# Kernel optimization log

Hardware: AMD Instinct MI355X
Metric: run time of the kernel (lower is better)

The kernel has to match this reference:

```python
import jax, jax.numpy as jnp
import numpy as np

N = 8192
IN_DIM = 512
OUT_DIM = 512


def setup_inputs() -> dict:
    key = jax.random.key(0)
    kA, kX, k1, k2, k3, k4 = jax.random.split(key, 6)
    A = jax.random.uniform(kA, (N, N), dtype=jnp.float32)  # strictly positive -> nonzero triu
    X = jax.random.normal(kX, (N, IN_DIM), dtype=jnp.float32)
    s = 1.0 / np.sqrt(IN_DIM)
    W1 = jax.random.uniform(k1, (OUT_DIM, IN_DIM), minval=-s, maxval=s, dtype=jnp.float32)  # fc
    b1 = jax.random.uniform(k2, (OUT_DIM,), minval=-s, maxval=s, dtype=jnp.float32)
    W2 = jax.random.uniform(k3, (OUT_DIM, IN_DIM), minval=-s, maxval=s, dtype=jnp.float32)  # fc2
    b2 = jax.random.uniform(k4, (OUT_DIM,), minval=-s, maxval=s, dtype=jnp.float32)
    return {"A": A, "X": X, "W1": W1, "b1": b1, "W2": W2, "b2": b2}


def reference(A, X, W1, b1, W2, b2):
    n = A.shape[0]
    # strictly upper-triangular mask (diagonal=1); with uniform(0,1) fill all these
    # entries are nonzero, so torch.nonzero selects exactly them: m = n(n-1)/2 values.
    triu_mask = jnp.triu(jnp.ones((n, n), dtype=bool), k=1)
    m = n * (n - 1) // 2
    # torch.median = lower median = sorted[(m-1)//2]; pad non-triu entries with +inf
    vals = jnp.where(triu_mask, A, jnp.inf).reshape(-1)
    median_value = jnp.sort(vals)[(m - 1) // 2]
    # A[A < median] = 0
    A_thr = jnp.where(A < median_value, jnp.zeros((), A.dtype), A)
    A_norm = jax.nn.softmax(A_thr, axis=-1)
    fcX = X @ W1.T + b1    # [N, out_dim]
    fc2X = X @ W2.T + b2   # [N, out_dim]
    out = jax.nn.leaky_relu(0.1 * fc2X + 0.9 * (A_norm @ fcX), negative_slope=0.01)
    return out
```

## Files before the change

kernel.cpp:

```cpp
#include <hip/hip_runtime.h>

#define DEVI __device__ __forceinline__

typedef __attribute__((ext_vector_type(8))) short short8;
typedef __attribute__((ext_vector_type(4))) float f32x4;

static constexpr int NN = 8192;
static constexpr int DD = 512;
static constexpr unsigned LOB = 0x3EFE0000u;
static constexpr unsigned HIB = 0x3F020000u;
static constexpr long long K_RANK = 16775167LL;

static constexpr size_t WS_HIST   = 0;
static constexpr size_t WS_CNT    = 1048576;
static constexpr size_t WS_MED    = 1048832;
static constexpr size_t WS_COARSE = 1049088;
static constexpr size_t WS_XB     = 2097152;
static constexpr size_t WS_W1B  = WS_XB  + (size_t)NN * DD * 2;
static constexpr size_t WS_W2B  = WS_W1B + (size_t)DD * DD * 2;
static constexpr size_t WS_FCXT = WS_W2B + (size_t)DD * DD * 2;
static constexpr size_t WS_FC2  = WS_FCXT + (size_t)NN * DD * 2;
static constexpr size_t WS_UP   = WS_FC2 + (size_t)NN * DD * 4;
static constexpr size_t WS_ZP   = WS_UP  + (size_t)4 * NN * DD * 2;

DEVI unsigned short f2bf(float f) {
  unsigned u = __float_as_uint(f);
  u += 0x7fffu + ((u >> 16) & 1u);
  return (unsigned short)(u >> 16);
}
DEVI float bf2f(unsigned short h) { return __uint_as_float(((unsigned)h) << 16); }
DEVI int swz(int row, int kq) { return kq ^ ((row >> 1) & 3); }

DEVI void gl_lds16(const void* g, void* l) {
  __builtin_amdgcn_global_load_lds(
      (const __attribute__((address_space(1))) unsigned*)g,
      (__attribute__((address_space(3))) unsigned*)l, 16, 0, 0);
}

#define VMCNT(n) asm volatile("s_waitcnt vmcnt(" #n ")" ::: "memory")
#define LGKM0 asm volatile("s_waitcnt lgkmcnt(0)" ::: "memory")

__global__ __launch_bounds__(256) void zero_k(uint4* __restrict__ hist4,
                                              unsigned* __restrict__ cntmed) {
  hist4[blockIdx.x * 256 + threadIdx.x] = (uint4){0u, 0u, 0u, 0u};
  if (blockIdx.x == 0 && threadIdx.x < 2) cntmed[threadIdx.x * 64] = 0u;
}


DEVI void convert_body(const float* __restrict__ X, const float* __restrict__ W1,
                       const float* __restrict__ W2, unsigned short* __restrict__ Xb,
                       unsigned short* __restrict__ W1b, unsigned short* __restrict__ W2b,
                       int cb, int tid) {
  const long long NX = (long long)NN * DD;
  const long long NW = (long long)DD * DD;
  const long long total4 = (NX + 2 * NW) / 4;
  for (long long q = (long long)cb * 512 + tid; q < total4; q += 65536LL) {
    long long e = q << 2;
    const float4* src; unsigned short* dst; long long off;
    if (e < NX)           { src = (const float4*)X;  dst = Xb;  off = e; }
    else if (e < NX + NW) { src = (const float4*)W1; dst = W1b; off = e - NX; }
    else                  { src = (const float4*)W2; dst = W2b; off = e - NX - NW; }
    float4 v = src[off >> 2];
    ushort4 o;
    o.x = f2bf(v.x); o.y = f2bf(v.y); o.z = f2bf(v.z); o.w = f2bf(v.w);
    *(ushort4*)(dst + off) = o;
  }
}

DEVI void hist_body(const float* __restrict__ A, unsigned* __restrict__ hist,
                    unsigned* __restrict__ below, int hb, int tid) {
  unsigned cnt = 0;
  const float4* A4 = (const float4*)A;
  const long long STR = 458752LL;
#pragma unroll 1
  for (long long q0 = (long long)hb * 512 + tid; q0 < 16777216LL; q0 += 8 * STR) {
    float4 v[8];
    int act = 0;
#pragma unroll
    for (int i = 0; i < 8; ++i) {
      long long qi = q0 + i * STR;
      if (qi < 16777216LL) {
        int row = (int)(qi >> 11);
        int col = (int)((qi & 2047) << 2);
        if (col + 3 > row) { act |= 1 << i; v[i] = A4[qi]; }
      }
    }
#pragma unroll
    for (int i = 0; i < 8; ++i) {
      if (act & (1 << i)) {
        long long qi = q0 + i * STR;
        int row = (int)(qi >> 11);
        int col = (int)((qi & 2047) << 2);
        float vv[4] = {v[i].x, v[i].y, v[i].z, v[i].w};
#pragma unroll
        for (int j = 0; j < 4; ++j) {
          if (col + j > row) {
            unsigned u = __float_as_uint(vv[j]);
            if (u < LOB) cnt++;
            else if (u < HIB) atomicAdd(&hist[u - LOB], 1u);
          }
        }
      }
    }
  }
  for (int off = 32; off > 0; off >>= 1) cnt += __shfl_down(cnt, off);
  if ((tid & 63) == 0 && cnt) atomicAdd(below, cnt);
}

__global__ __launch_bounds__(512) void stage1_k(const float* __restrict__ A,
                                                const float* __restrict__ X,
                                                const float* __restrict__ W1,
                                                const float* __restrict__ W2,
                                                unsigned* __restrict__ hist,
                                                unsigned* __restrict__ below,
                                                unsigned short* __restrict__ Xb,
                                                unsigned short* __restrict__ W1b,
                                                unsigned short* __restrict__ W2b) {
  const int bx = blockIdx.x;
  if (bx < 128) convert_body(X, W1, W2, Xb, W1b, W2b, bx, threadIdx.x);
  else          hist_body(A, hist, below, bx - 128, threadIdx.x);
}


template <bool BROW, bool OBF>
DEVI void gemm_small_body(const unsigned short* __restrict__ Am,
                          const unsigned short* __restrict__ Bm,
                          const float* __restrict__ bias, void* __restrict__ outp,
                          int ldout, int m0, int n0, char* apB, char* btB) {
  const int tid = threadIdx.x, lane = tid & 63, w = tid >> 6;
  const int wm = w >> 2, wn = w & 3;
  const int lr = lane & 15, lq = lane >> 4;
  const int rL = lane >> 2, kq = lane & 3;
  f32x4 acc[2][4];
#pragma unroll
  for (int i = 0; i < 2; ++i)
#pragma unroll
    for (int j = 0; j < 4; ++j) acc[i][j] = (f32x4){0.f, 0.f, 0.f, 0.f};

#pragma unroll 1
  for (int kt = 0; kt < 16; ++kt) {
    const int k0 = kt * 32;
    __syncthreads();
    if (w < 4) {
      int r = w * 16 + rL;
      gl_lds16(Am + ((size_t)(m0 + r) * DD + k0 + swz(r, kq) * 8), apB + w * 1024);
    }
#pragma unroll
    for (int i = 0; i < 2; ++i) {
      int blk = w * 2 + i;
      int r = blk * 16 + rL;
      gl_lds16(Bm + ((size_t)(n0 + r) * DD + k0 + swz(r, kq) * 8), btB + blk * 1024);
    }
    __syncthreads();
    short8 a[2], b[4];
#pragma unroll
    for (int fr = 0; fr < 2; ++fr) {
      int r = wm * 32 + fr * 16 + lr;
      a[fr] = *(const short8*)(apB + r * 64 + swz(r, lq) * 16);
    }
#pragma unroll
    for (int fc = 0; fc < 4; ++fc) {
      int r = wn * 64 + fc * 16 + lr;
      b[fc] = *(const short8*)(btB + r * 64 + swz(r, lq) * 16);
    }
#pragma unroll
    for (int fr = 0; fr < 2; ++fr)
#pragma unroll
      for (int fc = 0; fc < 4; ++fc)
        acc[fr][fc] = __builtin_amdgcn_mfma_f32_16x16x32_bf16(a[fr], b[fc], acc[fr][fc], 0, 0, 0);
  }
#pragma unroll
  for (int fr = 0; fr < 2; ++fr)
#pragma unroll
    for (int fc = 0; fc < 4; ++fc)
#pragma unroll
      for (int j = 0; j < 4; ++j) {
        int row = m0 + wm * 32 + fr * 16 + lq * 4 + j;
        int col = n0 + wn * 64 + fc * 16 + lr;
        float v = acc[fr][fc][j] + (BROW ? bias[row] : bias[col]);
        if (OBF) ((unsigned short*)outp)[(size_t)row * ldout + col] = f2bf(v);
        else     ((float*)outp)[(size_t)row * ldout + col] = v;
      }
}

__global__ __launch_bounds__(512, 2) void stage2_k(const unsigned short* __restrict__ Xb,
                                                   const unsigned short* __restrict__ W1b,
                                                   const unsigned short* __restrict__ W2b,
                                                   const float* __restrict__ b1,
                                                   const float* __restrict__ b2,
                                                   unsigned short* __restrict__ fcXT,
                                                   float* __restrict__ fc2,
                                                   const unsigned* __restrict__ hist,
                                                   unsigned* __restrict__ coarse) {
  __shared__ alignas(16) char plds[20480];
  const int bx = blockIdx.x;
  if (bx < 256) {
    int m0 = ((bx >> 3) & 7) * 64;
    int n0 = ((bx & 7) | ((bx >> 6) << 3)) * 256;
    gemm_small_body<true, true>(W1b, Xb, b1, (void*)fcXT, NN, m0, n0, plds, plds + 4096);
  } else if (bx < 512) {
    int q = bx - 256;
    gemm_small_body<false, false>(Xb, W2b, b2, (void*)fc2, DD,
                                  (q >> 1) * 64, (q & 1) * 256, plds, plds + 4096);
  } else {
    const int tid = threadIdx.x;
    const int half = tid >> 8;
    const int g = ((bx - 512) << 1) | half;
    unsigned v = hist[g * 256 + (tid & 255)];
    for (int off = 32; off > 0; off >>= 1) v += __shfl_down(v, off);
    unsigned* part = (unsigned*)plds;
    if ((tid & 63) == 0) part[tid >> 6] = v;
    __syncthreads();
    if ((tid & 255) == 0)
      coarse[g] = part[half * 4] + part[half * 4 + 1] + part[half * 4 + 2] + part[half * 4 + 3];
  }
}

__global__ __launch_bounds__(1024) void select_k(const unsigned* __restrict__ hist,
                                                 const unsigned* __restrict__ coarse,
                                                 const unsigned* __restrict__ below,
                                                 unsigned* __restrict__ med) {
  __shared__ unsigned ssum[1024];
  __shared__ int owner;
  __shared__ unsigned tg_s;
  const int t = threadIdx.x;
  unsigned own = coarse[t];
  ssum[t] = own;
  __syncthreads();
  for (int off = 1; off < 1024; off <<= 1) {
    unsigned v = (t >= off) ? ssum[t - off] : 0u;
    __syncthreads();
    ssum[t] += v;
    __syncthreads();
  }
  long long target = K_RANK - (long long)(*below);
  unsigned incl = ssum[t];
  unsigned excl = incl - own;
  if (target >= (long long)excl && target < (long long)incl) {
    owner = t;
    tg_s = (unsigned)(target - (long long)excl);
  }
  __syncthreads();
  const int to = owner;
  const unsigned tg = tg_s;
  unsigned v256 = (t < 256) ? hist[to * 256 + t] : 0u;
  __syncthreads();
  if (t < 256) ssum[t] = v256;
  __syncthreads();
  for (int off = 1; off < 256; off <<= 1) {
    unsigned v = (t < 256 && t >= off) ? ssum[t - off] : 0u;
    __syncthreads();
    if (t < 256) ssum[t] += v;
    __syncthreads();
  }
  if (t < 256) {
    unsigned incl2 = ssum[t];
    unsigned excl2 = incl2 - v256;
    if (tg >= excl2 && tg < incl2) *med = LOB + (unsigned)(to * 256 + t);
  }
}

static constexpr int LDS_A0 = 0;
static constexpr int LDS_A1 = 8192;
static constexpr int LDS_B0 = 16384;
static constexpr int LDS_B1 = 49152;

__global__ __launch_bounds__(512, 2) void main_gemm_k(const float* __restrict__ A,
                                                      const unsigned short* __restrict__ fcXT,
                                                      const unsigned* __restrict__ medp,
                                                      unsigned short* __restrict__ Up,
                                                      float* __restrict__ Zp) {
  __shared__ alignas(16) char lds[81920];
  const int tid = threadIdx.x, lane = tid & 63, w = tid >> 6;
  const int wm = w >> 2, wn = w & 3;
  const int lr = lane & 15, lq = lane >> 4;
  const int fid = blockIdx.x;
  const int xcd = fid & 7;
  const int ks = xcd >> 1;
  const int m0 = (((xcd & 1) << 5) | (fid >> 3)) << 7;
  const int kbase = ks * 2048;
  const float med = __uint_as_float(*medp);
  const int rB = lane >> 2, kqB = lane & 3;
  const int rA = tid >> 2, cqA = tid & 3;
  const float* aRow = A + (size_t)(m0 + rA) * NN;
  const int ldsAw = rA * 64 + swz(rA, cqA) * 16;

  float zacc = 0.f;
  f32x4 acc[4][8];
#pragma unroll
  for (int i = 0; i < 4; ++i)
#pragma unroll
    for (int j = 0; j < 8; ++j) acc[i][j] = (f32x4){0.f, 0.f, 0.f, 0.f};
  float4 vA00, vA01, vA10, vA11;

#define CONV8(V0, V1, DST)                                                     \
  {                                                                            \
    float vv[8] = {V0.x, V0.y, V0.z, V0.w, V1.x, V1.y, V1.z, V1.w};            \
    short8 pb;                                                                 \
    _Pragma("unroll")                                                          \
    for (int j = 0; j < 8; ++j) {                                              \
      float a_ = vv[j];                                                        \
      float p_ = (a_ < med) ? 1.0f : __expf(a_);                               \
      unsigned short h_ = f2bf(p_);                                            \
      pb[j] = (short)h_;                                                       \
      zacc += bf2f(h_);                                                        \
    }                                                                          \
    *(short8*)(DST) = pb;                                                      \
  }

  {
#pragma unroll
    for (int i = 0; i < 4; ++i) {
      int blk = w * 4 + i;
      int o = blk * 16 + rB;
      gl_lds16(fcXT + ((size_t)o * NN + kbase + swz(o, kqB) * 8), lds + LDS_B0 + blk * 1024);
    }
    const float* ap0 = aRow + kbase + cqA * 8;
    float4 t0 = *(const float4*)ap0;
    float4 t1 = *(const float4*)(ap0 + 4);
    vA00 = *(const float4*)(ap0 + 32);
    vA01 = *(const float4*)(ap0 + 36);
    CONV8(t0, t1, lds + LDS_A0 + ldsAw);
  }
  __syncthreads();

#define ITER(KT, CUR, NCUR, VAC0, VAC1, VAN0, VAN1)                            \
  {                                                                            \
    const int kt_ = (KT);                                                      \
    if (kt_ < 63) {                                                            \
      const int k1 = kbase + (kt_ + 1) * 32;                                   \
      _Pragma("unroll")                                                        \
      for (int i = 0; i < 4; ++i) {                                            \
        int blk = w * 4 + i;                                                   \
        int o = blk * 16 + rB;                                                 \
        gl_lds16(fcXT + ((size_t)o * NN + k1 + swz(o, kqB) * 8),               \
                 lds + LDS_B##NCUR + blk * 1024);                              \
      }                                                                        \
      if (kt_ < 62) {                                                          \
        const float* apf = aRow + kbase + (kt_ + 2) * 32 + cqA * 8;            \
        asm volatile("global_load_dwordx4 %0, %2, off\n\t"                     \
                     "global_load_dwordx4 %1, %2, off offset:16"               \
                     : "=&v"(VAN0), "=&v"(VAN1)                                \
                     : "v"(apf)                                                \
                     : "memory");                                              \
      }                                                                        \
    }                                                                          \
    short8 af[4], bfr[8];                                                      \
    _Pragma("unroll")                                                          \
    for (int fr = 0; fr < 4; ++fr) {                                           \
      int r = wm * 64 + fr * 16 + lr;                                          \
      af[fr] = *(const short8*)(lds + LDS_A##CUR + r * 64 + swz(r, lq) * 16);  \
    }                                                                          \
    _Pragma("unroll")                                                          \
    for (int fc = 0; fc < 8; ++fc) {                                           \
      int o = wn * 128 + fc * 16 + lr;                                         \
      bfr[fc] = *(const short8*)(lds + LDS_B##CUR + o * 64 + swz(o, lq) * 16); \
    }                                                                          \
    __builtin_amdgcn_s_setprio(1);                                             \
    _Pragma("unroll")                                                          \
    for (int fr = 0; fr < 4; ++fr)                                             \
      _Pragma("unroll")                                                        \
      for (int fc = 0; fc < 8; ++fc)                                           \
        acc[fr][fc] = __builtin_amdgcn_mfma_f32_16x16x32_bf16(af[fr], bfr[fc], \
                                                              acc[fr][fc], 0, 0, 0); \
    __builtin_amdgcn_s_setprio(0);                                             \
    if (kt_ < 63) {                                                            \
      if (kt_ < 62) { VMCNT(6); } else { VMCNT(4); }                           \
      __builtin_amdgcn_sched_barrier(0);                                       \
      CONV8(VAC0, VAC1, lds + LDS_A##NCUR + ldsAw);                            \
      if (kt_ < 62) { VMCNT(2); } else { VMCNT(0); }                           \
      LGKM0;                                                                   \
      __builtin_amdgcn_s_barrier();                                            \
    }                                                                          \
  }

#pragma unroll 1
  for (int t2 = 0; t2 < 32; ++t2) {
    ITER(2 * t2,     0, 1, vA00, vA01, vA10, vA11);
    ITER(2 * t2 + 1, 1, 0, vA10, vA11, vA00, vA01);
  }
#undef ITER
#undef CONV8

  zacc += __shfl_xor(zacc, 1);
  zacc += __shfl_xor(zacc, 2);
  if ((lane & 3) == 0) Zp[(size_t)ks * NN + m0 + rA] = zacc;
#pragma unroll
  for (int fr = 0; fr < 4; ++fr)
#pragma unroll
    for (int fc = 0; fc < 8; ++fc)
#pragma unroll
      for (int j = 0; j < 4; ++j) {
        int row = m0 + wm * 64 + fr * 16 + lq * 4 + j;
        int col = wn * 128 + fc * 16 + lr;
        Up[((size_t)ks << 22) + ((size_t)row << 9) + col] = f2bf(acc[fr][fc][j]);
      }
}

__global__ __launch_bounds__(256) void reduce_k(const unsigned short* __restrict__ Up,
                                                const float* __restrict__ Zp,
                                                const float* __restrict__ fc2,
                                                float* __restrict__ out) {
  long long t = (long long)blockIdx.x * blockDim.x + threadIdx.x;
  if (t >= (long long)NN * DD / 8) return;
  long long base = t << 3;
  int row = (int)(base >> 9);
  float Z = Zp[row] + Zp[NN + row] + Zp[2 * NN + row] + Zp[3 * NN + row];
  float inv = 0.9f / Z;
  float s[8] = {0, 0, 0, 0, 0, 0, 0, 0};
#pragma unroll
  for (int sp = 0; sp < 4; ++sp) {
    const uint4 u = *(const uint4*)(Up + ((long long)sp << 22) + base);
    const unsigned uu[4] = {u.x, u.y, u.z, u.w};
#pragma unroll
    for (int j = 0; j < 4; ++j) {
      s[2 * j]     += __uint_as_float(uu[j] << 16);
      s[2 * j + 1] += __uint_as_float(uu[j] & 0xffff0000u);
    }
  }
  float4 fa = *(const float4*)(fc2 + base);
  float4 fb = *(const float4*)(fc2 + base + 4);
  float fv[8] = {fa.x, fa.y, fa.z, fa.w, fb.x, fb.y, fb.z, fb.w};
  float o[8];
#pragma unroll
  for (int j = 0; j < 8; ++j) {
    float v = 0.1f * fv[j] + inv * s[j];
    o[j] = v >= 0.f ? v : 0.01f * v;
  }
  *(float4*)(out + base)     = (float4){o[0], o[1], o[2], o[3]};
  *(float4*)(out + base + 4) = (float4){o[4], o[5], o[6], o[7]};
}

extern "C" void kernel_launch(void* const* d_in, const int* in_sizes, int n_in,
                              void* d_out, int out_size, void* d_ws, size_t ws_size,
                              hipStream_t stream) {
  const float* A  = (const float*)d_in[0];
  const float* X  = (const float*)d_in[1];
  const float* W1 = (const float*)d_in[2];
  const float* b1 = (const float*)d_in[3];
  const float* W2 = (const float*)d_in[4];
  const float* b2 = (const float*)d_in[5];
  char* ws = (char*)d_ws;
  unsigned* hist   = (unsigned*)(ws + WS_HIST);
  unsigned* cnt    = (unsigned*)(ws + WS_CNT);
  unsigned* med    = (unsigned*)(ws + WS_MED);
  unsigned* coarse = (unsigned*)(ws + WS_COARSE);
  unsigned short* Xb   = (unsigned short*)(ws + WS_XB);
  unsigned short* W1b  = (unsigned short*)(ws + WS_W1B);
  unsigned short* W2b  = (unsigned short*)(ws + WS_W2B);
  unsigned short* fcXT = (unsigned short*)(ws + WS_FCXT);
  float* fc2           = (float*)(ws + WS_FC2);
  unsigned short* Upp  = (unsigned short*)(ws + WS_UP);
  float* Zp            = (float*)(ws + WS_ZP);

  hipLaunchKernelGGL(zero_k, dim3(256), dim3(256), 0, stream, (uint4*)hist, cnt);
  hipLaunchKernelGGL(stage1_k, dim3(1024), dim3(512), 0, stream,
                     A, X, W1, W2, hist, cnt, Xb, W1b, W2b);
  hipLaunchKernelGGL(stage2_k, dim3(1024), dim3(512), 0, stream,
                     Xb, W1b, W2b, b1, b2, fcXT, fc2, hist, coarse);
  hipLaunchKernelGGL(select_k, dim3(1), dim3(1024), 0, stream, hist, coarse, cnt, med);
  hipLaunchKernelGGL(main_gemm_k, dim3(256), dim3(512), 0, stream, A, fcXT, med, Upp, Zp);
  hipLaunchKernelGGL(reduce_k, dim3(2048), dim3(256), 0, stream, Upp, Zp, fc2, (float*)d_out);
}
```

Measured before the change: 237.2 us.

## Double K-tile to 64 per stage and drop register-prefetched A pipeline

Each main-loop stage now covers two 32-wide K sub-steps: B is staged into LDS for 64 columns at a time and A is loaded and converted into two LDS sub-tiles. This halves the number of barriers and loop iterations. In exchange, the two-ahead register prefetch of A and the hand-placed vmcnt waits are removed, so A global-load latency now sits right after the MFMA phase. LDS per block doubles to 160 KB, which likely stops two blocks from fitting on a CU.

```diff
diff --git a/kernel.cpp b/kernel.cpp
--- a/kernel.cpp
+++ b/kernel.cpp
@@ -36,9 +36,6 @@
       (const __attribute__((address_space(1))) unsigned*)g,
       (__attribute__((address_space(3))) unsigned*)l, 16, 0, 0);
 }
-
-#define VMCNT(n) asm volatile("s_waitcnt vmcnt(" #n ")" ::: "memory")
-#define LGKM0 asm volatile("s_waitcnt lgkmcnt(0)" ::: "memory")
 
 __global__ __launch_bounds__(256) void zero_k(uint4* __restrict__ hist4,
                                               unsigned* __restrict__ cntmed) {
@@ -261,16 +258,16 @@
 }
 
 static constexpr int LDS_A0 = 0;
-static constexpr int LDS_A1 = 8192;
-static constexpr int LDS_B0 = 16384;
-static constexpr int LDS_B1 = 49152;
+static constexpr int LDS_A1 = 16384;
+static constexpr int LDS_B0 = 32768;
+static constexpr int LDS_B1 = 98304;
 
 __global__ __launch_bounds__(512, 2) void main_gemm_k(const float* __restrict__ A,
                                                       const unsigned short* __restrict__ fcXT,
                                                       const unsigned* __restrict__ medp,
                                                       unsigned short* __restrict__ Up,
                                                       float* __restrict__ Zp) {
-  __shared__ alignas(16) char lds[81920];
+  __shared__ alignas(16) char lds[163840];
   const int tid = threadIdx.x, lane = tid & 63, w = tid >> 6;
   const int wm = w >> 2, wn = w & 3;
   const int lr = lane & 15, lq = lane >> 4;
@@ -291,7 +288,6 @@
   for (int i = 0; i < 4; ++i)
 #pragma unroll
     for (int j = 0; j < 8; ++j) acc[i][j] = (f32x4){0.f, 0.f, 0.f, 0.f};
-  float4 vA00, vA01, vA10, vA11;
 
 #define CONV8(V0, V1, DST)                                                     \
   {                                                                            \
@@ -308,78 +304,75 @@
     *(short8*)(DST) = pb;                                                      \
   }
 
-  {
-#pragma unroll
-    for (int i = 0; i < 4; ++i) {
-      int blk = w * 4 + i;
-      int o = blk * 16 + rB;
-      gl_lds16(fcXT + ((size_t)o * NN + kbase + swz(o, kqB) * 8), lds + LDS_B0 + blk * 1024);
-    }
-    const float* ap0 = aRow + kbase + cqA * 8;
-    float4 t0 = *(const float4*)ap0;
-    float4 t1 = *(const float4*)(ap0 + 4);
-    vA00 = *(const float4*)(ap0 + 32);
-    vA01 = *(const float4*)(ap0 + 36);
-    CONV8(t0, t1, lds + LDS_A0 + ldsAw);
-  }
+#define STAGE_B(KOFF, BBASE)                                                   \
+  _Pragma("unroll")                                                            \
+  for (int s = 0; s < 2; ++s) {                                                \
+    _Pragma("unroll")                                                          \
+    for (int i = 0; i < 4; ++i) {                                              \
+      int blk = w * 4 + i;                                                     \
+      int o = blk * 16 + rB;                                                   \
+      gl_lds16(fcXT + ((size_t)o * NN + (KOFF) + s * 32 + swz(o, kqB) * 8),    \
+               lds + (BBASE) + s * 32768 + blk * 1024);                        \
+    }                                                                          \
+  }
+
+#define LOAD_CONV_A(KOFF, ABASE)                                               \
+  {                                                                            \
+    const float* ap_ = aRow + (KOFF) + cqA * 8;                                \
+    float4 t0_ = *(const float4*)ap_;                                          \
+    float4 t1_ = *(const float4*)(ap_ + 4);                                    \
+    float4 t2_ = *(const float4*)(ap_ + 32);                                   \
+    float4 t3_ = *(const float4*)(ap_ + 36);                                   \
+    CONV8(t0_, t1_, lds + (ABASE) + ldsAw);                                    \
+    CONV8(t2_, t3_, lds + (ABASE) + 8192 + ldsAw);                             \
+  }
+
+  STAGE_B(kbase, LDS_B0);
+  LOAD_CONV_A(kbase, LDS_A0);
   __syncthreads();
 
-#define ITER(KT, CUR, NCUR, VAC0, VAC1, VAN0, VAN1)                            \
+#define ITER(KT, CUR, NCUR)                                                    \
   {                                                                            \
     const int kt_ = (KT);                                                      \
-    if (kt_ < 63) {                                                            \
-      const int k1 = kbase + (kt_ + 1) * 32;                                   \
+    if (kt_ < 31) { STAGE_B(kbase + (kt_ + 1) * 64, LDS_B##NCUR); }            \
+    _Pragma("unroll")                                                          \
+    for (int ksb = 0; ksb < 2; ++ksb) {                                        \
+      short8 af[4], bfr[8];                                                    \
       _Pragma("unroll")                                                        \
-      for (int i = 0; i < 4; ++i) {                                            \
-        int blk = w * 4 + i;                                                   \
-        int o = blk * 16 + rB;                                                 \
-        gl_lds16(fcXT + ((size_t)o * NN + k1 + swz(o, kqB) * 8),               \
-                 lds + LDS_B##NCUR + blk * 1024);                              \
+      for (int fr = 0; fr < 4; ++fr) {                                         \
+        int r = wm * 64 + fr * 16 + lr;                                        \
+        af[fr] = *(const short8*)(lds + LDS_A##CUR + ksb * 8192 +              \
+                                  r * 64 + swz(r, lq) * 16);                   \
       }                                                                        \
-      if (kt_ < 62) {                                                          \
-        const float* apf = aRow + kbase + (kt_ + 2) * 32 + cqA * 8;            \
-        asm volatile("global_load_dwordx4 %0, %2, off\n\t"                     \
-                     "global_load_dwordx4 %1, %2, off offset:16"               \
-                     : "=&v"(VAN0), "=&v"(VAN1)                                \
-                     : "v"(apf)                                                \
-                     : "memory");                                              \
+      _Pragma("unroll")                                                        \
+      for (int fc = 0; fc < 8; ++fc) {                                         \
+        int o = wn * 128 + fc * 16 + lr;                                       \
+        bfr[fc] = *(const short8*)(lds + LDS_B##CUR + ksb * 32768 +            \
+                                   o * 64 + swz(o, lq) * 16);                  \
       }                                                                        \
+      __builtin_amdgcn_s_setprio(1);                                           \
+      _Pragma("unroll")                                                        \
+      for (int fr = 0; fr < 4; ++fr)                                           \
+        _Pragma("unroll")                                                      \
+        for (int fc = 0; fc < 8; ++fc)                                         \
+          acc[fr][fc] = __builtin_amdgcn_mfma_f32_16x16x32_bf16(               \
+              af[fr], bfr[fc], acc[fr][fc], 0, 0, 0);                          \
+      __builtin_amdgcn_s_setprio(0);                                           \
     }                                                                          \
-    short8 af[4], bfr[8];                                                      \
-    _Pragma("unroll")                                                          \
-    for (int fr = 0; fr < 4; ++fr) {                                           \
-      int r = wm * 64 + fr * 16 + lr;                                          \
-      af[fr] = *(const short8*)(lds + LDS_A##CUR + r * 64 + swz(r, lq) * 16);  \
+    if (kt_ < 31) {                                                            \
+      LOAD_CONV_A(kbase + (kt_ + 1) * 64, LDS_A##NCUR);                        \
+      __syncthreads();                                                         \
     }                                                                          \
-    _Pragma("unroll")                                                          \
-    for (int fc = 0; fc < 8; ++fc) {                                           \
-      int o = wn * 128 + fc * 16 + lr;                                         \
-      bfr[fc] = *(const short8*)(lds + LDS_B##CUR + o * 64 + swz(o, lq) * 16); \
-    }                                                                          \
-    __builtin_amdgcn_s_setprio(1);                                             \
-    _Pragma("unroll")                                                          \
-    for (int fr = 0; fr < 4; ++fr)                                             \
-      _Pragma("unroll")                                                        \
-      for (int fc = 0; fc < 8; ++fc)                                           \
-        acc[fr][fc] = __builtin_amdgcn_mfma_f32_16x16x32_bf16(af[fr], bfr[fc], \
-                                                              acc[fr][fc], 0, 0, 0); \
-    __builtin_amdgcn_s_setprio(0);                                             \
-    if (kt_ < 63) {                                                            \
-      if (kt_ < 62) { VMCNT(6); } else { VMCNT(4); }                           \
-      __builtin_amdgcn_sched_barrier(0);                                       \
-      CONV8(VAC0, VAC1, lds + LDS_A##NCUR + ldsAw);                            \
-      if (kt_ < 62) { VMCNT(2); } else { VMCNT(0); }                           \
-      LGKM0;                                                                   \
-      __builtin_amdgcn_s_barrier();                                            \
-    }                                                                          \
   }
 
 #pragma unroll 1
-  for (int t2 = 0; t2 < 32; ++t2) {
-    ITER(2 * t2,     0, 1, vA00, vA01, vA10, vA11);
-    ITER(2 * t2 + 1, 1, 0, vA10, vA11, vA00, vA01);
+  for (int t2 = 0; t2 < 16; ++t2) {
+    ITER(2 * t2,     0, 1);
+    ITER(2 * t2 + 1, 1, 0);
   }
 #undef ITER
+#undef LOAD_CONV_A
+#undef STAGE_B
 #undef CONV8
 
   zacc += __shfl_xor(zacc, 1);
```

Measured after the change: 305.6 us. 28.9% more time.
